# Kernel tuning notes

Measured on AMD Instinct MI355X. Metric: run time of the kernel, lower is better.

## Reference

```python
import jax, jax.numpy as jnp
import numpy as np

B, T, W, HP = 1, 64, 88, 48   # batch, frames, pitches, hidden_per_pitch
NU, NH, K = 24, 4, 25          # n_unit, n_heads, neighborhood window
HD = NU // NH                  # head dim = 6
HL = NU // 2                   # LSTM hidden per direction = 12


def _lstm_bidir(x, w_ih, w_hh, b_ih, b_hh):
    # x: [N, T, In]; w_ih: [2, 4*HL, In]; w_hh: [2, 4*HL, HL]; biases: [2, 4*HL]
    N = x.shape[0]
    def run(Wih, Whh, bih, bhh, reverse):
        def step(carry, xt):
            h, c = carry
            g = xt @ Wih.T + h @ Whh.T + bih + bhh
            i, f, gg, o = jnp.split(g, 4, axis=-1)  # torch gate order i,f,g,o
            c = jax.nn.sigmoid(f) * c + jax.nn.sigmoid(i) * jnp.tanh(gg)
            h = jax.nn.sigmoid(o) * jnp.tanh(c)
            return (h, c), h
        init = (jnp.zeros((N, HL), x.dtype), jnp.zeros((N, HL), x.dtype))
        _, ys = jax.lax.scan(step, init, jnp.swapaxes(x, 0, 1), reverse=reverse)
        return jnp.swapaxes(ys, 0, 1)
    return jnp.concatenate([run(w_ih[0], w_hh[0], b_ih[0], b_hh[0], False),
                            run(w_ih[1], w_hh[1], b_ih[1], b_hh[1], True)], axis=-1)


def _natten2d(x, qkv_w, qkv_b, rpb, proj_w, proj_b):
    # Neighborhood attention over 2D grid [B, Hh, Ww] with KxK window clamped at borders.
    Bn, Hh, Ww, C = x.shape
    qkv = (x @ qkv_w.T + qkv_b).reshape(Bn, Hh, Ww, 3, NH, HD)
    q = qkv[..., 0, :, :] * (HD ** -0.5)
    k = qkv[..., 1, :, :]
    v = qkv[..., 2, :, :]
    half = K // 2
    ar = jnp.arange(K)
    idx_i = jnp.clip(jnp.arange(Hh) - half, 0, Hh - K)[:, None] + ar  # [Hh,K]
    idx_j = jnp.clip(jnp.arange(Ww) - half, 0, Ww - K)[:, None] + ar  # [Ww,K]
    kg = k[:, idx_i][:, :, :, idx_j]  # [B,Hh,K,Ww,K,NH,HD]
    vg = v[:, idx_i][:, :, :, idx_j]
    ri = idx_i - jnp.arange(Hh)[:, None] + (K - 1)  # relative pos bias indices [Hh,K]
    rj = idx_j - jnp.arange(Ww)[:, None] + (K - 1)  # [Ww,K]
    bias = rpb[:, ri][:, :, :, rj]                  # [NH,Hh,K,Ww,K]
    logits = jnp.einsum('bijnd,biajcnd->bnijac', q, kg)
    logits = logits + jnp.transpose(bias, (0, 1, 3, 2, 4))[None]
    attn = jax.nn.softmax(logits.reshape(Bn, NH, Hh, Ww, K * K), axis=-1)
    attn = attn.reshape(Bn, NH, Hh, Ww, K, K)
    out = jnp.einsum('bnijac,biajcnd->bijnd', attn, vg).reshape(Bn, Hh, Ww, C)
    return out @ proj_w.T + proj_b


def _forward(features, condition, mask, emb, w_ih_l0, w_hh_l0, b_ih_l0, b_hh_l0,
             w_ih_l1, w_hh_l1, b_ih_l1, b_hh_l1, qkv_w, qkv_b, rpb, proj_w, proj_b,
             out_w, out_b):
    # concat: [B,T,88,HP] + [B,T,88,4] + [B,T,88,1] -> [B,T,88,HP+5]
    cat = jnp.concatenate([jnp.transpose(features, (0, 1, 3, 2)), emb[condition],
                           mask[..., None]], axis=-1)
    x = jnp.transpose(cat, (0, 2, 1, 3)).reshape(B * W, T, HP + 5)  # pitchwise LSTM
    x = _lstm_bidir(x, w_ih_l0, w_hh_l0, b_ih_l0, b_hh_l0)
    x = _lstm_bidir(x, w_ih_l1, w_hh_l1, b_ih_l1, b_hh_l1)
    x = jnp.transpose(x.reshape(B, W, T, NU), (0, 2, 1, 3))  # [B,T,88,NU]
    for _ in range(2):  # n_layers=2; Sequential(*[m]*2) => SHARED weights
        x = _natten2d(x, qkv_w, qkv_b, rpb, proj_w, proj_b)
    return x @ out_w.T + out_b  # [B,T,88,5]


def setup_inputs():
    ks = jax.random.split(jax.random.key(0), 24)
    def unif(k, shape, fan):
        s = 1.0 / np.sqrt(fan)
        return jax.random.uniform(k, shape, jnp.float32, -s, s)
    return {
        'features': jax.random.normal(ks[0], (B, T, HP, W), jnp.float32),
        'condition': jax.random.randint(ks[1], (B, T, W), 0, 5),
        'mask': jax.random.uniform(ks[2], (B, T, W), jnp.float32),
        'emb': jax.random.normal(ks[3], (5, 4), jnp.float32),
        'w_ih_l0': unif(ks[4], (2, 4 * HL, HP + 5), HL),
        'w_hh_l0': unif(ks[5], (2, 4 * HL, HL), HL),
        'b_ih_l0': unif(ks[6], (2, 4 * HL), HL),
        'b_hh_l0': unif(ks[7], (2, 4 * HL), HL),
        'w_ih_l1': unif(ks[8], (2, 4 * HL, 2 * HL), HL),
        'w_hh_l1': unif(ks[9], (2, 4 * HL, HL), HL),
        'b_ih_l1': unif(ks[10], (2, 4 * HL), HL),
        'b_hh_l1': unif(ks[11], (2, 4 * HL), HL),
        'qkv_w': unif(ks[12], (3 * NU, NU), NU),
        'qkv_b': unif(ks[13], (3 * NU,), NU),
        'rpb': jax.random.normal(ks[14], (NH, 2 * K - 1, 2 * K - 1), jnp.float32) * 0.02,
        'proj_w': unif(ks[15], (NU, NU), NU),
        'proj_b': unif(ks[16], (NU,), NU),
        'out_w': unif(ks[17], (5, NU), NU),
        'out_b': unif(ks[18], (5,), NU),
    }


def reference(features, condition, mask, emb, w_ih_l0, w_hh_l0, b_ih_l0, b_hh_l0,
              w_ih_l1, w_hh_l1, b_ih_l1, b_hh_l1, qkv_w, qkv_b, rpb, proj_w, proj_b,
              out_w, out_b):
    return _forward(features, condition, mask, emb, w_ih_l0, w_hh_l0, b_ih_l0, b_hh_l0,
                    w_ih_l1, w_hh_l1, b_ih_l1, b_hh_l1, qkv_w, qkv_b, rpb,
                    proj_w, proj_b, out_w, out_b)
```

## Files before the change

### kernel.cpp

```cpp
#include <hip/hip_runtime.h>
#include <hip/hip_bf16.h>

#define NPIX (64*88)
#define NSEQ 88
#define TT 64
#define F0 53
#define GATES 48

typedef __hip_bfloat16 bf16;

__device__ __forceinline__ float frcp(float x){ return __builtin_amdgcn_rcpf(x); }

__device__ __forceinline__ void unpack6(uint4 r, float* f){
  f[0] = __uint_as_float(r.x << 16);
  f[1] = __uint_as_float(r.x & 0xffff0000u);
  f[2] = __uint_as_float(r.y << 16);
  f[3] = __uint_as_float(r.y & 0xffff0000u);
  f[4] = __uint_as_float(r.z << 16);
  f[5] = __uint_as_float(r.z & 0xffff0000u);
}

__global__ __launch_bounds__(256) void k_core(
    const float* __restrict__ feat, const int* __restrict__ cond,
    const float* __restrict__ mask, const float* __restrict__ emb,
    const float* __restrict__ wih0, const float* __restrict__ whh0,
    const float* __restrict__ bih0, const float* __restrict__ bhh0,
    const float* __restrict__ wih1, const float* __restrict__ whh1,
    const float* __restrict__ bih1, const float* __restrict__ bhh1,
    const float* __restrict__ qkv_w, const float* __restrict__ qkv_b,
    float* __restrict__ q, bf16* __restrict__ kh, bf16* __restrict__ vh){
  int n = blockIdx.x; int tid = threadIdx.x;
  int wave = tid >> 6; int lane = tid & 63;
  __shared__ float smem[14816];
  float* gbuf = smem;
  float* sx   = smem + 6144;
  float* sw0  = smem + 6144+3392;
  float* w1   = smem + 6144;
  float* sqkv = smem + 6144+2400;
  float* y0   = smem + 6144+4200;
  float* y1   = smem + 6144+5736;
  float* bsum = smem + 14624;

  for (int idx = tid; idx < 2*GATES*F0; idx += 256) sw0[idx] = wih0[idx];
  for (int idx = tid; idx < TT*F0; idx += 256){
    int t = idx / F0, f = idx - t*F0;
    float v;
    if (f < 48)      v = feat[(t*48 + f)*88 + n];
    else if (f < 52) v = emb[cond[t*88+n]*4 + (f-48)];
    else             v = mask[t*88+n];
    sx[idx] = v;
  }
  if (tid < 96)       bsum[tid] = bih0[tid] + bhh0[tid];
  else if (tid < 192) bsum[tid] = bih1[tid-96] + bhh1[tid-96];
  __syncthreads();

  for (int r = 0; r < 24; ++r){
    int row = tid + r*256;
    int d = row / 3072; int rem = row - d*3072;
    int t = rem / 48; int j = rem - t*48;
    const float* xr = sx + t*F0;
    const float* wr = sw0 + (d*GATES + j)*F0;
    float a0=0.f, a1=0.f, a2=0.f, a3=0.f;
    #pragma unroll
    for (int f=0; f<52; f+=4){
      a0 += xr[f  ]*wr[f  ];
      a1 += xr[f+1]*wr[f+1];
      a2 += xr[f+2]*wr[f+2];
      a3 += xr[f+3]*wr[f+3];
    }
    gbuf[(d*TT + t)*GATES + j] = bsum[d*GATES+j] + xr[52]*wr[52] + ((a0+a1)+(a2+a3));
  }
  __syncthreads();

  if (wave >= 2){
    for (int idx = tid-128; idx < 2*GATES*24; idx += 128){
      int row = idx / 24, f = idx - row*24;
      w1[row*25 + f] = wih1[idx];
    }
    for (int idx = tid-128; idx < 72*24; idx += 128){
      int row = idx / 24, f = idx - row*24;
      sqkv[row*25 + f] = qkv_w[idx];
    }
  } else {
    int d = wave;
    int j = (lane < GATES) ? lane : (lane - GATES);
    int u = j % 12; int grp = j / 12;
    float w[12];
    const float* wb = whh0 + (d*GATES + j)*12;
    #pragma unroll
    for (int m=0;m<12;++m) w[m] = wb[m];
    float negs  = (grp==2) ? -2.f : -1.f;
    float amul  = (grp==2) ?  2.f :  1.f;
    float aadd  = (grp==2) ? -1.f :  0.f;
    const float* gb = gbuf + d*TT*GATES + j;
    float hval = 0.f, cval = 0.f;
    int t0 = d ? (TT-1) : 0;
    float gnext = gb[t0*GATES];
    for (int s=0;s<TT;++s){
      int t = d ? (TT-1-s) : s;
      float gg = gnext;
      int tn = d ? max(TT-2-s,0) : min(s+1,TT-1);
      gnext = gb[tn*GATES];
      float h0=__shfl(hval,0), h1=__shfl(hval,1), h2=__shfl(hval,2);
      float h3=__shfl(hval,3), h4=__shfl(hval,4), h5=__shfl(hval,5);
      float h6=__shfl(hval,6), h7=__shfl(hval,7), h8=__shfl(hval,8);
      float h9=__shfl(hval,9), h10=__shfl(hval,10), h11=__shfl(hval,11);
      float a0 = gg + h0*w[0] + h4*w[4] + h8*w[8];
      float a1 = h1*w[1] + h5*w[5] + h9*w[9];
      float a2 = h2*w[2] + h6*w[6] + h10*w[10];
      float a3 = h3*w[3] + h7*w[7] + h11*w[11];
      float dot = (a0+a1)+(a2+a3);
      float act = amul*frcp(1.f + __expf(negs*dot)) + aadd;
      float ai = __shfl(act, u);
      float af = __shfl(act, u+12);
      float ag = __shfl(act, u+24);
      float ao = __shfl(act, u+36);
      float cn = af*cval + ai*ag;
      float th = 2.f*frcp(1.f + __expf(-2.f*cn)) - 1.f;
      hval = ao*th; cval = cn;
      if (lane < 12) y0[t*24 + d*12 + lane] = hval;
    }
  }
  __syncthreads();

  for (int r = 0; r < 24; ++r){
    int row = tid + r*256;
    int d = row / 3072; int rem = row - d*3072;
    int t = rem / 48; int j = rem - t*48;
    const float* xr = y0 + t*24;
    const float* wr = w1 + (d*GATES + j)*25;
    float a0=0.f, a1=0.f;
    #pragma unroll
    for (int c=0; c<24; c+=2){ a0 += xr[c]*wr[c]; a1 += xr[c+1]*wr[c+1]; }
    gbuf[(d*TT + t)*GATES + j] = bsum[96 + d*GATES+j] + a0 + a1;
  }
  __syncthreads();

  if (wave < 2){
    int d = wave;
    int j = (lane < GATES) ? lane : (lane - GATES);
    int u = j % 12; int grp = j / 12;
    float w[12];
    const float* wb = whh1 + (d*GATES + j)*12;
    #pragma unroll
    for (int m=0;m<12;++m) w[m] = wb[m];
    float negs  = (grp==2) ? -2.f : -1.f;
    float amul  = (grp==2) ?  2.f :  1.f;
    float aadd  = (grp==2) ? -1.f :  0.f;
    const float* gb = gbuf + d*TT*GATES + j;
    float hval = 0.f, cval = 0.f;
    int t0 = d ? (TT-1) : 0;
    float gnext = gb[t0*GATES];
    for (int s=0;s<TT;++s){
      int t = d ? (TT-1-s) : s;
      float gg = gnext;
      int tn = d ? max(TT-2-s,0) : min(s+1,TT-1);
      gnext = gb[tn*GATES];
      float h0=__shfl(hval,0), h1=__shfl(hval,1), h2=__shfl(hval,2);
      float h3=__shfl(hval,3), h4=__shfl(hval,4), h5=__shfl(hval,5);
      float h6=__shfl(hval,6), h7=__shfl(hval,7), h8=__shfl(hval,8);
      float h9=__shfl(hval,9), h10=__shfl(hval,10), h11=__shfl(hval,11);
      float a0 = gg + h0*w[0] + h4*w[4] + h8*w[8];
      float a1 = h1*w[1] + h5*w[5] + h9*w[9];
      float a2 = h2*w[2] + h6*w[6] + h10*w[10];
      float a3 = h3*w[3] + h7*w[7] + h11*w[11];
      float dot = (a0+a1)+(a2+a3);
      float act = amul*frcp(1.f + __expf(negs*dot)) + aadd;
      float ai = __shfl(act, u);
      float af = __shfl(act, u+12);
      float ag = __shfl(act, u+24);
      float ao = __shfl(act, u+36);
      float cn = af*cval + ai*ag;
      float th = 2.f*frcp(1.f + __expf(-2.f*cn)) - 1.f;
      hval = ao*th; cval = cn;
      if (lane < 12) y1[t*24 + d*12 + lane] = hval;
    }
  }
  __syncthreads();

  for (int r = 0; r < 18; ++r){
    int idx = tid + r*256;
    int gq = idx % 72; int t = idx / 72;
    int p = t*88 + n;
    const float* xr = y1 + t*24;
    const float* wr = sqkv + gq*25;
    float a0=0.f, a1=0.f;
    #pragma unroll
    for (int c=0; c<24; c+=2){ a0 += xr[c]*wr[c]; a1 += xr[c+1]*wr[c+1]; }
    float acc = qkv_b[gq] + a0 + a1;
    int s = gq/24, rem = gq - s*24;
    if (s==0) q[p*24+rem] = acc*0.4082482904638631f;
    else {
      int hh = rem/6, pos = rem - hh*6;
      bf16* dst = (s==1) ? kh : vh;
      dst[((size_t)hh*NPIX + p)*8 + pos] = __float2bfloat16(acc);
    }
  }
}

__global__ __launch_bounds__(256) void k_attn_fused(
    const float* __restrict__ q, const bf16* __restrict__ kh,
    const bf16* __restrict__ vh, const float* __restrict__ rpb,
    const float* __restrict__ pw, const float* __restrict__ pb,
    const float* __restrict__ qkv_w, const float* __restrict__ qkv_b,
    float* __restrict__ q2, bf16* __restrict__ kh2, bf16* __restrict__ vh2,
    const float* __restrict__ ow, const float* __restrict__ ob,
    float* __restrict__ out, int last){
  int p = blockIdx.x; int tid = threadIdx.x;
  int h = tid >> 6; int lane = tid & 63;
  int i = p / 88, j = p - i*88;
  int si = min(max(i-12,0),39), sj = min(max(j-12,0),63);
  __shared__ float aorow[24];
  __shared__ float xrow[24];

  float qv[6];
  #pragma unroll
  for (int d=0; d<6; ++d) qv[d] = q[p*24 + h*6 + d];
  const uint4* kb = (const uint4*)(kh + (size_t)h*NPIX*8);
  const uint4* vb = (const uint4*)(vh + (size_t)h*NPIX*8);
  float lgv[10]; int roff[10];
  float lmax = -1e30f;
  #pragma unroll
  for (int it=0; it<10; ++it){
    int nb = lane + it*64;
    bool valid = nb < 625;
    int nbc = valid ? nb : 624;
    int a = nbc/25, cc = nbc - a*25;
    int gi = si + a, gj = sj + cc;
    int row = gi*88+gj;
    roff[it] = row;
    float kr[6];
    unpack6(kb[row], kr);
    float lg = qv[0]*kr[0]+qv[1]*kr[1]+qv[2]*kr[2]+qv[3]*kr[3]+qv[4]*kr[4]+qv[5]*kr[5];
    lg += rpb[(h*49 + (gi - i + 24))*49 + (gj - j + 24)];
    lg = valid ? lg : -1e30f;
    lgv[it] = lg;
    lmax = fmaxf(lmax, lg);
  }
  #pragma unroll
  for (int off=32; off; off>>=1) lmax = fmaxf(lmax, __shfl_xor(lmax, off));
  float lsum = 0.f;
  #pragma unroll
  for (int it=0; it<10; ++it){
    float pe = __expf(lgv[it]-lmax);
    lgv[it] = pe; lsum += pe;
  }
  #pragma unroll
  for (int off=32; off; off>>=1) lsum += __shfl_xor(lsum, off);
  float acc[6] = {0,0,0,0,0,0};
  #pragma unroll
  for (int it=0; it<10; ++it){
    float vr[6];
    unpack6(vb[roff[it]], vr);
    float pe = lgv[it];
    #pragma unroll
    for (int d=0; d<6; ++d) acc[d] += pe*vr[d];
  }
  #pragma unroll
  for (int d=0; d<6; ++d){
    #pragma unroll
    for (int off=32; off; off>>=1) acc[d] += __shfl_xor(acc[d], off);
  }
  if (lane == 0){
    float inv = 1.f/lsum;
    #pragma unroll
    for (int d=0; d<6; ++d) aorow[h*6+d] = acc[d]*inv;
  }
  __syncthreads();

  if (tid < 24){
    float a2 = pb[tid];
    const float* wr = pw + tid*24;
    #pragma unroll
    for (int c=0;c<24;++c) a2 += aorow[c]*wr[c];
    xrow[tid] = a2;
  }
  __syncthreads();

  if (!last){
    if (tid < 72){
      float a2 = qkv_b[tid];
      const float* wr = qkv_w + tid*24;
      #pragma unroll
      for (int c=0;c<24;++c) a2 += xrow[c]*wr[c];
      int s = tid/24, rem = tid - s*24;
      if (s==0) q2[p*24+rem] = a2*0.4082482904638631f;
      else {
        int hh = rem/6, pos = rem - hh*6;
        bf16* dst = (s==1) ? kh2 : vh2;
        dst[((size_t)hh*NPIX + p)*8 + pos] = __float2bfloat16(a2);
      }
    }
  } else {
    if (tid < 5){
      float a2 = ob[tid];
      const float* wr = ow + tid*24;
      #pragma unroll
      for (int c=0;c<24;++c) a2 += xrow[c]*wr[c];
      out[p*5+tid] = a2;
    }
  }
}

extern "C" void kernel_launch(void* const* d_in, const int* in_sizes, int n_in,
                              void* d_out, int out_size, void* d_ws, size_t ws_size,
                              hipStream_t stream) {
  const float* feat    = (const float*)d_in[0];
  const int*   cond    = (const int*)  d_in[1];
  const float* mask    = (const float*)d_in[2];
  const float* emb     = (const float*)d_in[3];
  const float* w_ih_l0 = (const float*)d_in[4];
  const float* w_hh_l0 = (const float*)d_in[5];
  const float* b_ih_l0 = (const float*)d_in[6];
  const float* b_hh_l0 = (const float*)d_in[7];
  const float* w_ih_l1 = (const float*)d_in[8];
  const float* w_hh_l1 = (const float*)d_in[9];
  const float* b_ih_l1 = (const float*)d_in[10];
  const float* b_hh_l1 = (const float*)d_in[11];
  const float* qkv_w   = (const float*)d_in[12];
  const float* qkv_b   = (const float*)d_in[13];
  const float* rpb     = (const float*)d_in[14];
  const float* proj_w  = (const float*)d_in[15];
  const float* proj_b  = (const float*)d_in[16];
  const float* out_w   = (const float*)d_in[17];
  const float* out_b   = (const float*)d_in[18];
  float* out = (float*)d_out;

  float* ws  = (float*)d_ws;
  float* Q1  = ws;
  float* Q2  = Q1 + 135168;
  bf16*  KH1 = (bf16*)(Q2 + 135168);
  bf16*  VH1 = KH1 + 180224;
  bf16*  KH2 = VH1 + 180224;
  bf16*  VH2 = KH2 + 180224;

  k_core<<<NSEQ, 256, 0, stream>>>(
      feat, cond, mask, emb,
      w_ih_l0, w_hh_l0, b_ih_l0, b_hh_l0,
      w_ih_l1, w_hh_l1, b_ih_l1, b_hh_l1,
      qkv_w, qkv_b, Q1, KH1, VH1);

  k_attn_fused<<<NPIX, 256, 0, stream>>>(
      Q1, KH1, VH1, rpb, proj_w, proj_b, qkv_w, qkv_b,
      Q2, KH2, VH2, out_w, out_b, out, 0);

  k_attn_fused<<<NPIX, 256, 0, stream>>>(
      Q2, KH2, VH2, rpb, proj_w, proj_b, qkv_w, qkv_b,
      Q1, KH1, VH1, out_w, out_b, out, 1);
}
```

Measured before the change: 214.0 us.

## Tile neighborhood attention with shared-memory K/V staging and split projection kernels

The attention kernel now processes a 4x2 tile of query pixels per head in each block. It stages the union of their K/V neighborhoods (28x26) in LDS, so the heavily overlapping windows are no longer re-read from global memory per pixel. The projection and qkv/output GEMVs move into separate small kernels, and attention outputs now make a round trip through a workspace buffer. k_core also goes from 256 to 1024 threads to widen its parallel phases, at the cost of extra launches and extra global traffic for the AO buffer.

```diff
diff --git a/kernel.cpp b/kernel.cpp
--- a/kernel.cpp
+++ b/kernel.cpp
@@ -20,7 +20,7 @@
   f[5] = __uint_as_float(r.z & 0xffff0000u);
 }
 
-__global__ __launch_bounds__(256) void k_core(
+__global__ __launch_bounds__(1024) void k_core(
     const float* __restrict__ feat, const int* __restrict__ cond,
     const float* __restrict__ mask, const float* __restrict__ emb,
     const float* __restrict__ wih0, const float* __restrict__ whh0,
@@ -41,8 +41,8 @@
   float* y1   = smem + 6144+5736;
   float* bsum = smem + 14624;
 
-  for (int idx = tid; idx < 2*GATES*F0; idx += 256) sw0[idx] = wih0[idx];
-  for (int idx = tid; idx < TT*F0; idx += 256){
+  for (int idx = tid; idx < 2*GATES*F0; idx += 1024) sw0[idx] = wih0[idx];
+  for (int idx = tid; idx < TT*F0; idx += 1024){
     int t = idx / F0, f = idx - t*F0;
     float v;
     if (f < 48)      v = feat[(t*48 + f)*88 + n];
@@ -54,8 +54,9 @@
   else if (tid < 192) bsum[tid] = bih1[tid-96] + bhh1[tid-96];
   __syncthreads();
 
-  for (int r = 0; r < 24; ++r){
-    int row = tid + r*256;
+  #pragma unroll
+  for (int r = 0; r < 6; ++r){
+    int row = tid + r*1024;
     int d = row / 3072; int rem = row - d*3072;
     int t = rem / 48; int j = rem - t*48;
     const float* xr = sx + t*F0;
@@ -73,11 +74,11 @@
   __syncthreads();
 
   if (wave >= 2){
-    for (int idx = tid-128; idx < 2*GATES*24; idx += 128){
+    for (int idx = tid-128; idx < 2*GATES*24; idx += 896){
       int row = idx / 24, f = idx - row*24;
       w1[row*25 + f] = wih1[idx];
     }
-    for (int idx = tid-128; idx < 72*24; idx += 128){
+    for (int idx = tid-128; idx < 72*24; idx += 896){
       int row = idx / 24, f = idx - row*24;
       sqkv[row*25 + f] = qkv_w[idx];
     }
@@ -123,8 +124,9 @@
   }
   __syncthreads();
 
-  for (int r = 0; r < 24; ++r){
-    int row = tid + r*256;
+  #pragma unroll
+  for (int r = 0; r < 6; ++r){
+    int row = tid + r*1024;
     int d = row / 3072; int rem = row - d*3072;
     int t = rem / 48; int j = rem - t*48;
     const float* xr = y0 + t*24;
@@ -178,8 +180,7 @@
   }
   __syncthreads();
 
-  for (int r = 0; r < 18; ++r){
-    int idx = tid + r*256;
+  for (int idx = tid; idx < TT*72; idx += 1024){
     int gq = idx % 72; int t = idx / 72;
     int p = t*88 + n;
     const float* xr = y1 + t*24;
@@ -198,27 +199,44 @@
   }
 }
 
-__global__ __launch_bounds__(256) void k_attn_fused(
+__global__ __launch_bounds__(512) void k_attn(
     const float* __restrict__ q, const bf16* __restrict__ kh,
     const bf16* __restrict__ vh, const float* __restrict__ rpb,
-    const float* __restrict__ pw, const float* __restrict__ pb,
-    const float* __restrict__ qkv_w, const float* __restrict__ qkv_b,
-    float* __restrict__ q2, bf16* __restrict__ kh2, bf16* __restrict__ vh2,
-    const float* __restrict__ ow, const float* __restrict__ ob,
-    float* __restrict__ out, int last){
-  int p = blockIdx.x; int tid = threadIdx.x;
-  int h = tid >> 6; int lane = tid & 63;
-  int i = p / 88, j = p - i*88;
-  int si = min(max(i-12,0),39), sj = min(max(j-12,0),63);
-  __shared__ float aorow[24];
-  __shared__ float xrow[24];
+    float* __restrict__ ao){
+  int b = blockIdx.x;
+  int h = b / 704; int rem = b - h*704;
+  int ti = rem / 44, tj = rem - ti*44;
+  int i0 = ti*4, j0 = tj*2;
+  int tid = threadIdx.x;
+  int w = tid >> 6; int lane = tid & 63;
+  int osi = min(max(i0-12,0),39);
+  int osj = min(max(j0-12,0),63);
+
+  __shared__ uint4 kt[28*26];
+  __shared__ uint4 vt[28*26];
+  const uint4* kg = (const uint4*)(kh + (size_t)h*NPIX*8);
+  const uint4* vg = (const uint4*)(vh + (size_t)h*NPIX*8);
+  for (int idx = tid; idx < 28*26; idx += 512){
+    int a = idx / 26, cc = idx - a*26;
+    int gi = min(osi + a, 63), gj = min(osj + cc, 87);
+    int src = gi*88 + gj;
+    kt[idx] = kg[src];
+    vt[idx] = vg[src];
+  }
+  __syncthreads();
+
+  int pi = i0 + (w>>1), pj = j0 + (w&1);
+  int p = pi*88 + pj;
+  int dsi = min(max(pi-12,0),39) - osi;
+  int dsj = min(max(pj-12,0),63) - osj;
+  int rbi = osi + dsi - pi + 24;
+  int rbj = osj + dsj - pj + 24;
 
   float qv[6];
   #pragma unroll
   for (int d=0; d<6; ++d) qv[d] = q[p*24 + h*6 + d];
-  const uint4* kb = (const uint4*)(kh + (size_t)h*NPIX*8);
-  const uint4* vb = (const uint4*)(vh + (size_t)h*NPIX*8);
-  float lgv[10]; int roff[10];
+
+  float lgv[10]; int rof[10];
   float lmax = -1e30f;
   #pragma unroll
   for (int it=0; it<10; ++it){
@@ -226,13 +244,12 @@
     bool valid = nb < 625;
     int nbc = valid ? nb : 624;
     int a = nbc/25, cc = nbc - a*25;
-    int gi = si + a, gj = sj + cc;
-    int row = gi*88+gj;
-    roff[it] = row;
+    int r = (a+dsi)*26 + (cc+dsj);
+    rof[it] = r;
     float kr[6];
-    unpack6(kb[row], kr);
+    unpack6(kt[r], kr);
     float lg = qv[0]*kr[0]+qv[1]*kr[1]+qv[2]*kr[2]+qv[3]*kr[3]+qv[4]*kr[4]+qv[5]*kr[5];
-    lg += rpb[(h*49 + (gi - i + 24))*49 + (gj - j + 24)];
+    lg += rpb[(h*49 + (a + rbi))*49 + (cc + rbj)];
     lg = valid ? lg : -1e30f;
     lgv[it] = lg;
     lmax = fmaxf(lmax, lg);
@@ -251,7 +268,7 @@
   #pragma unroll
   for (int it=0; it<10; ++it){
     float vr[6];
-    unpack6(vb[roff[it]], vr);
+    unpack6(vt[rof[it]], vr);
     float pe = lgv[it];
     #pragma unroll
     for (int d=0; d<6; ++d) acc[d] += pe*vr[d];
@@ -262,43 +279,67 @@
     for (int off=32; off; off>>=1) acc[d] += __shfl_xor(acc[d], off);
   }
   if (lane == 0){
-    float inv = 1.f/lsum;
-    #pragma unroll
-    for (int d=0; d<6; ++d) aorow[h*6+d] = acc[d]*inv;
-  }
-  __syncthreads();
-
+    float inv = frcp(lsum);
+    #pragma unroll
+    for (int d=0; d<6; ++d) ao[p*24 + h*6 + d] = acc[d]*inv;
+  }
+}
+
+__global__ __launch_bounds__(64) void k_proj_qkv(const float* __restrict__ ain,
+    const float* __restrict__ pw, const float* __restrict__ pb,
+    const float* __restrict__ qkv_w, const float* __restrict__ qkv_b,
+    float* __restrict__ q2, bf16* __restrict__ kh2, bf16* __restrict__ vh2){
+  int p = blockIdx.x; int tid = threadIdx.x;
+  __shared__ float arow[24];
+  __shared__ float xrow[24];
+  if (tid < 24) arow[tid] = ain[p*24+tid];
+  __syncthreads();
   if (tid < 24){
     float a2 = pb[tid];
     const float* wr = pw + tid*24;
     #pragma unroll
-    for (int c=0;c<24;++c) a2 += aorow[c]*wr[c];
+    for (int c=0;c<24;++c) a2 += arow[c]*wr[c];
     xrow[tid] = a2;
   }
   __syncthreads();
-
-  if (!last){
-    if (tid < 72){
-      float a2 = qkv_b[tid];
-      const float* wr = qkv_w + tid*24;
-      #pragma unroll
-      for (int c=0;c<24;++c) a2 += xrow[c]*wr[c];
-      int s = tid/24, rem = tid - s*24;
-      if (s==0) q2[p*24+rem] = a2*0.4082482904638631f;
-      else {
-        int hh = rem/6, pos = rem - hh*6;
-        bf16* dst = (s==1) ? kh2 : vh2;
-        dst[((size_t)hh*NPIX + p)*8 + pos] = __float2bfloat16(a2);
-      }
-    }
-  } else {
-    if (tid < 5){
-      float a2 = ob[tid];
-      const float* wr = ow + tid*24;
-      #pragma unroll
-      for (int c=0;c<24;++c) a2 += xrow[c]*wr[c];
-      out[p*5+tid] = a2;
-    }
+  for (int g = tid; g < 72; g += 64){
+    float a2 = qkv_b[g];
+    const float* wr = qkv_w + g*24;
+    #pragma unroll
+    for (int c=0;c<24;++c) a2 += xrow[c]*wr[c];
+    int s = g/24, rem = g - s*24;
+    if (s==0) q2[p*24+rem] = a2*0.4082482904638631f;
+    else {
+      int hh = rem/6, pos = rem - hh*6;
+      bf16* dst = (s==1) ? kh2 : vh2;
+      dst[((size_t)hh*NPIX + p)*8 + pos] = __float2bfloat16(a2);
+    }
+  }
+}
+
+__global__ __launch_bounds__(64) void k_proj_out(const float* __restrict__ ain,
+    const float* __restrict__ pw, const float* __restrict__ pb,
+    const float* __restrict__ ow, const float* __restrict__ ob,
+    float* __restrict__ out){
+  int p = blockIdx.x; int tid = threadIdx.x;
+  __shared__ float arow[24];
+  __shared__ float xrow[24];
+  if (tid < 24) arow[tid] = ain[p*24+tid];
+  __syncthreads();
+  if (tid < 24){
+    float a2 = pb[tid];
+    const float* wr = pw + tid*24;
+    #pragma unroll
+    for (int c=0;c<24;++c) a2 += arow[c]*wr[c];
+    xrow[tid] = a2;
+  }
+  __syncthreads();
+  if (tid < 5){
+    float a2 = ob[tid];
+    const float* wr = ow + tid*24;
+    #pragma unroll
+    for (int c=0;c<24;++c) a2 += xrow[c]*wr[c];
+    out[p*5+tid] = a2;
   }
 }
 
@@ -329,22 +370,24 @@
   float* ws  = (float*)d_ws;
   float* Q1  = ws;
   float* Q2  = Q1 + 135168;
-  bf16*  KH1 = (bf16*)(Q2 + 135168);
+  float* AO  = Q2 + 135168;
+  bf16*  KH1 = (bf16*)(AO + 135168);
   bf16*  VH1 = KH1 + 180224;
   bf16*  KH2 = VH1 + 180224;
   bf16*  VH2 = KH2 + 180224;
 
-  k_core<<<NSEQ, 256, 0, stream>>>(
+  k_core<<<NSEQ, 1024, 0, stream>>>(
       feat, cond, mask, emb,
       w_ih_l0, w_hh_l0, b_ih_l0, b_hh_l0,
       w_ih_l1, w_hh_l1, b_ih_l1, b_hh_l1,
       qkv_w, qkv_b, Q1, KH1, VH1);
 
-  k_attn_fused<<<NPIX, 256, 0, stream>>>(
-      Q1, KH1, VH1, rpb, proj_w, proj_b, qkv_w, qkv_b,
-      Q2, KH2, VH2, out_w, out_b, out, 0);
-
-  k_attn_fused<<<NPIX, 256, 0, stream>>>(
-      Q2, KH2, VH2, rpb, proj_w, proj_b, qkv_w, qkv_b,
-      Q1, KH1, VH1, out_w, out_b, out, 1);
-}
+  k_attn<<<4*16*44, 512, 0, stream>>>(Q1, KH1, VH1, rpb, AO);
+
+  k_proj_qkv<<<NPIX, 64, 0, stream>>>(AO, proj_w, proj_b, qkv_w, qkv_b,
+                                      Q2, KH2, VH2);
+
+  k_attn<<<4*16*44, 512, 0, stream>>>(Q2, KH2, VH2, rpb, AO);
+
+  k_proj_out<<<NPIX, 64, 0, stream>>>(AO, proj_w, proj_b, out_w, out_b, out);
+}
```

Measured after the change: 210.3 us. No clear change (-1.7%).
